# Kernel tuning notes

Measured on AMD Instinct MI355X. Metric: run time of the kernel, lower is better.

Reference implementation:

```python
import jax, jax.numpy as jnp
import numpy as np

H = 4                 # num_heads
GATE_NORM = 16.0      # gate_logit_normalizer
EPS = 1e-5            # RMSNorm eps


def setup_inputs() -> dict:
    key = jax.random.key(0)
    ks = jax.random.split(key, 12)
    B, T, D = 8, 4096, 1024
    Dk_total, Dv_total, Dlow = D // 2, D, 16

    def w(k, shape, fan_in):
        return jax.random.normal(k, shape, dtype=jnp.float32) * (fan_in ** -0.5)

    return {
        "x": jax.random.normal(ks[0], (B, T, D), dtype=jnp.float32),
        "Wq": w(ks[1], (D, Dk_total), D),
        "Wk": w(ks[2], (D, Dk_total), D),
        "Wv": w(ks[3], (D, Dv_total), D),
        "gk_w1": w(ks[4], (D, Dlow), D),
        "gk_w2": w(ks[5], (Dlow, Dk_total), Dlow),
        "gk_b2": jnp.zeros((Dk_total,), dtype=jnp.float32),
        "Wg": w(ks[6], (D, Dv_total), D),
        "g_norm_w": jnp.ones((Dv_total // H,), dtype=jnp.float32),
        "Wo": w(ks[7], (Dv_total, D), Dv_total),
    }


def _gla_forward(x, Wq, Wk, Wv, gk_w1, gk_w2, gk_b2, Wg, g_norm_w, Wo):
    B, T, D = x.shape
    Dk = Wq.shape[1] // H
    Dv = Wv.shape[1] // H

    q = (x @ Wq).reshape(B, T, H, Dk) * (Dk ** -0.5)
    k = (x @ Wk).reshape(B, T, H, Dk)
    v = (x @ Wv).reshape(B, T, H, Dv)
    # low-rank gate logits -> log-space decay gk (<= 0)
    gk = jax.nn.log_sigmoid((x @ gk_w1) @ gk_w2 + gk_b2) / GATE_NORM
    gk = gk.reshape(B, T, H, Dk)

    # recurrent gated linear attention:
    #   S_t = exp(gk_t)[:, None] * S_{t-1} + k_t^T v_t ;  o_t = q_t @ S_t
    def step(S, qkvg):
        qt, kt, vt, gt = qkvg          # each [B, H, Dk|Dv]
        S = jnp.exp(gt)[..., None] * S + kt[..., None] * vt[..., None, :]
        ot = jnp.einsum("bhk,bhkv->bhv", qt, S)
        return S, ot

    S0 = jnp.zeros((B, H, Dk, Dv), dtype=x.dtype)
    tm = lambda a: jnp.swapaxes(a, 0, 1)  # [B,T,...] -> [T,B,...]
    _, o = jax.lax.scan(step, S0, (tm(q), tm(k), tm(v), tm(gk)))
    o = jnp.swapaxes(o, 0, 1)            # [B, T, H, Dv]

    # output gate: RMSNorm(o) * swish(g), per head
    g = (x @ Wg).reshape(B, T, H, Dv)
    o = o * jax.lax.rsqrt(jnp.mean(o * o, axis=-1, keepdims=True) + EPS) * g_norm_w
    o = o * (g * jax.nn.sigmoid(g))
    return o.reshape(B, T, H * Dv) @ Wo


def reference(x, Wq, Wk, Wv, gk_w1, gk_w2, gk_b2, Wg, g_norm_w, Wo):
    return _gla_forward(x, Wq, Wk, Wv, gk_w1, gk_w2, gk_b2, Wg, g_norm_w, Wo)
```

## Files before the change

### kernel.cpp

```cpp
#include <hip/hip_runtime.h>
#include <hip/hip_bf16.h>
#include <cstdint>
#include <cstddef>

typedef __hip_bfloat16 bf16;
typedef __attribute__((ext_vector_type(8))) short short8;
typedef __attribute__((ext_vector_type(4))) float floatx4;

__device__ __forceinline__ void gload_lds16(const void* g, void* l) {
  __builtin_amdgcn_global_load_lds(
      (__attribute__((address_space(1))) void*)(uintptr_t)g,
      (__attribute__((address_space(3))) void*)l, 16, 0, 0);
}

__device__ __forceinline__ short f2bbits(float f) {
  bf16 h = __float2bfloat16(f);
  return __builtin_bit_cast(short, h);
}
__device__ __forceinline__ float b2f(short s) {
  return __bfloat162float(__builtin_bit_cast(bf16, s));
}

__global__ __launch_bounds__(256) void convert_x(const float* __restrict__ x,
                                                 bf16* __restrict__ xb) {
  size_t i = ((size_t)blockIdx.x * 256 + threadIdx.x) * 8;
  float4 f0 = *(const float4*)(x + i);
  float4 f1 = *(const float4*)(x + i + 4);
  short8 r;
  r[0] = f2bbits(f0.x); r[1] = f2bbits(f0.y); r[2] = f2bbits(f0.z); r[3] = f2bbits(f0.w);
  r[4] = f2bbits(f1.x); r[5] = f2bbits(f1.y); r[6] = f2bbits(f1.z); r[7] = f2bbits(f1.w);
  *(short8*)(xb + i) = r;
}

__global__ __launch_bounds__(256) void transpose_w(const float* __restrict__ src,
                                                   bf16* __restrict__ dst, int cols) {
  __shared__ float tile[32][33];
  int n0 = blockIdx.x * 32, k0 = blockIdx.y * 32;
  int tx = threadIdx.x & 31, ty = threadIdx.x >> 5;
#pragma unroll
  for (int i = 0; i < 32; i += 8) {
    int kk = k0 + ty + i, nn = n0 + tx;
    tile[ty + i][tx] = (nn < cols) ? src[(size_t)kk * cols + nn] : 0.0f;
  }
  __syncthreads();
#pragma unroll
  for (int i = 0; i < 32; i += 8) {
    int nn = n0 + ty + i, kk = k0 + tx;
    if (nn < cols) dst[(size_t)nn * 1024 + kk] = __float2bfloat16(tile[tx][ty + i]);
  }
}

__global__ __launch_bounds__(256, 2) void gemm128(
    const bf16* __restrict__ A, const bf16* __restrict__ Bt, int K, int mode,
    float* __restrict__ oq, float* __restrict__ okk, bf16* __restrict__ ov,
    bf16* __restrict__ ogg, float* __restrict__ oo) {
  __shared__ __align__(16) bf16 sA[128 * 32];
  __shared__ __align__(16) bf16 sB[128 * 32];
  const int tid = threadIdx.x;
  const int wave = tid >> 6, lane = tid & 63;
  const int n0 = blockIdx.x * 128, m0 = blockIdx.y * 128;
  const int wm = (wave & 1) * 64, wn = (wave >> 1) * 64;
  const int srow = lane >> 2, scol = (lane & 3) * 8;
  floatx4 acc[4][4] = {};
  const int kIters = K >> 5;
  for (int kt = 0; kt < kIters; ++kt) {
    if (kt) __syncthreads();
    const int kO = (kt << 5) + scol;
#pragma unroll
    for (int c2 = 0; c2 < 2; ++c2) {
      const int chunk = wave * 2 + c2;
      gload_lds16(A + (size_t)(m0 + chunk * 16 + srow) * K + kO, &sA[chunk * 512]);
      gload_lds16(Bt + (size_t)(n0 + chunk * 16 + srow) * K + kO, &sB[chunk * 512]);
    }
    __syncthreads();
    const int l15 = lane & 15, q8 = (lane >> 4) * 8;
    short8 af[4], bfr[4];
#pragma unroll
    for (int i = 0; i < 4; ++i) af[i] = *(const short8*)&sA[(wm + i * 16 + l15) * 32 + q8];
#pragma unroll
    for (int j = 0; j < 4; ++j) bfr[j] = *(const short8*)&sB[(wn + j * 16 + l15) * 32 + q8];
#pragma unroll
    for (int i = 0; i < 4; ++i)
#pragma unroll
      for (int j = 0; j < 4; ++j)
        acc[i][j] = __builtin_amdgcn_mfma_f32_16x16x32_bf16(af[i], bfr[j], acc[i][j], 0, 0, 0);
  }
  const int l15 = lane & 15, rq = (lane >> 4) * 4;
#pragma unroll
  for (int i = 0; i < 4; ++i) {
#pragma unroll
    for (int j = 0; j < 4; ++j) {
      const int n = n0 + wn + j * 16 + l15;
#pragma unroll
      for (int r = 0; r < 4; ++r) {
        const int m = m0 + wm + i * 16 + rq + r;
        const float val = acc[i][j][r];
        if (mode == 1) {
          oo[(size_t)m * 1024 + n] = val;
        } else {
          if (n < 512)       oq[(size_t)m * 512 + n] = val * 0.08838834764831845f;
          else if (n < 1024) okk[(size_t)m * 512 + (n - 512)] = val;
          else if (n < 2048) ov[(size_t)m * 1024 + (n - 1024)] = __float2bfloat16(val);
          else               ogg[(size_t)m * 1024 + (n - 2048)] = __float2bfloat16(val);
        }
      }
    }
  }
}

__global__ __launch_bounds__(256) void gate_decay2(const float* __restrict__ x,
                                                   const float* __restrict__ w1,
                                                   const float* __restrict__ w2,
                                                   const float* __restrict__ b2,
                                                   float* __restrict__ gkout) {
  __shared__ float sp[256];
  __shared__ float sz[16];
  const int m = blockIdx.x, tid = threadIdx.x;
  const int j = tid & 15, dpart = tid >> 4;
  const float* xr = x + (size_t)m * 1024 + dpart * 64;
  float acc = 0.f;
#pragma unroll 8
  for (int e = 0; e < 64; ++e) acc = fmaf(xr[e], w1[(dpart * 64 + e) * 16 + j], acc);
  sp[tid] = acc;
  __syncthreads();
  if (tid < 16) {
    float s = 0.f;
#pragma unroll
    for (int p = 0; p < 16; ++p) s += sp[p * 16 + tid];
    sz[tid] = s;
  }
  __syncthreads();
#pragma unroll
  for (int u = 0; u < 2; ++u) {
    const int n = tid + u * 256;
    float t = b2[n];
#pragma unroll
    for (int jj = 0; jj < 16; ++jj) t = fmaf(sz[jj], w2[jj * 512 + n], t);
    const float ls = fminf(t, 0.f) - log1pf(__expf(-fabsf(t)));
    gkout[(size_t)m * 512 + n] = ls * 0.0625f;
  }
}

__global__ __launch_bounds__(128) void chunk_prep(
    const float* __restrict__ q, const float* __restrict__ k,
    const float* __restrict__ gk, bf16* __restrict__ qt,
    bf16* __restrict__ kt, float* __restrict__ dtot) {
  const int cid = blockIdx.x;
  const int c = cid & 63, h = (cid >> 6) & 3, b = cid >> 8;
  const int d = threadIdx.x;
  const size_t rowbase = ((size_t)(b * 4096 + c * 64)) * 512 + h * 128 + d;
  const size_t obase = (size_t)cid * 8192 + d;
  float bsum = 0.f;
  for (int i = 0; i < 64; ++i) {
    const size_t src = rowbase + (size_t)i * 512;
    bsum += gk[src];
    qt[obase + (size_t)i * 128] = __float2bfloat16(q[src] * __expf(bsum));
    kt[obase + (size_t)i * 128] = __float2bfloat16(k[src] * __expf(-bsum));
  }
  dtot[cid * 128 + d] = __expf(bsum);
}

__global__ __launch_bounds__(256) void chunk_intra(
    const bf16* __restrict__ qt, const bf16* __restrict__ kt,
    const float* __restrict__ dtot, const bf16* __restrict__ v,
    bf16* __restrict__ oi, bf16* __restrict__ ut) {
  __shared__ __align__(16) short lA[64 * 72];
  __shared__ __align__(16) short stg[27648];
  short* sQ = stg;
  short* sK = stg + 8704;
  short* sVT = stg;
  short* sKhT = stg + 18432;
  const int cid = blockIdx.x;
  const int c = cid & 63, h = (cid >> 6) & 3, b = cid >> 8;
  const int tid = threadIdx.x, wv = tid >> 6, lane = tid & 63;
  const int l15 = lane & 15, q8 = (lane >> 4) * 8, rq = (lane >> 4) * 4;

  {
    const int row = tid >> 2, seg = (tid & 3) * 32;
    const size_t src = (size_t)cid * 8192 + row * 128 + seg;
    const short8* qs = (const short8*)(qt + src);
    const short8* ks = (const short8*)(kt + src);
    short8* qd = (short8*)&sQ[row * 136 + seg];
    short8* kd = (short8*)&sK[row * 136 + seg];
#pragma unroll
    for (int t = 0; t < 4; ++t) { qd[t] = qs[t]; kd[t] = ks[t]; }
  }
  __syncthreads();
  {
    short8 af[4];
#pragma unroll
    for (int kf = 0; kf < 4; ++kf)
      af[kf] = *(const short8*)&sQ[(wv * 16 + l15) * 136 + kf * 32 + q8];
#pragma unroll
    for (int nt = 0; nt < 4; ++nt) {
      floatx4 accA = {0.f, 0.f, 0.f, 0.f};
#pragma unroll
      for (int kf = 0; kf < 4; ++kf) {
        short8 bfr = *(const short8*)&sK[(nt * 16 + l15) * 136 + kf * 32 + q8];
        accA = __builtin_amdgcn_mfma_f32_16x16x32_bf16(af[kf], bfr, accA, 0, 0, 0);
      }
#pragma unroll
      for (int r = 0; r < 4; ++r) {
        const int i = wv * 16 + rq + r, jj = nt * 16 + l15;
        lA[i * 72 + jj] = f2bbits(jj <= i ? accA[r] : 0.f);
      }
    }
  }
  __syncthreads();
  {
#pragma unroll
    for (int e = 0; e < 8; ++e) {
      const int idx = tid + e * 256;
      const int jj = idx >> 5, n0 = (idx & 31) * 8;
      short8 vv = *(const short8*)(v + ((size_t)(b * 4096 + c * 64 + jj)) * 1024 + h * 256 + n0);
#pragma unroll
      for (int t = 0; t < 8; ++t) sVT[(n0 + t) * 72 + jj] = vv[t];
    }
#pragma unroll
    for (int e = 0; e < 4; ++e) {
      const int idx = tid + e * 256;
      const int jj = idx >> 4, d0 = (idx & 15) * 8;
      short8 kk = *(const short8*)(kt + (size_t)cid * 8192 + jj * 128 + d0);
#pragma unroll
      for (int t = 0; t < 8; ++t)
        sKhT[(d0 + t) * 72 + jj] = f2bbits(b2f(kk[t]) * dtot[cid * 128 + d0 + t]);
    }
  }
  __syncthreads();
  {
    short8 aA0 = *(const short8*)&lA[(wv * 16 + l15) * 72 + q8];
    short8 aA1 = *(const short8*)&lA[(wv * 16 + l15) * 72 + 32 + q8];
#pragma unroll
    for (int nt = 0; nt < 16; ++nt) {
      short8 b0 = *(const short8*)&sVT[(nt * 16 + l15) * 72 + q8];
      short8 b1 = *(const short8*)&sVT[(nt * 16 + l15) * 72 + 32 + q8];
      floatx4 acc = {0.f, 0.f, 0.f, 0.f};
      acc = __builtin_amdgcn_mfma_f32_16x16x32_bf16(aA0, b0, acc, 0, 0, 0);
      acc = __builtin_amdgcn_mfma_f32_16x16x32_bf16(aA1, b1, acc, 0, 0, 0);
#pragma unroll
      for (int r = 0; r < 4; ++r) {
        const int i = wv * 16 + rq + r;
        oi[(size_t)cid * 16384 + i * 256 + nt * 16 + l15] = __builtin_bit_cast(bf16, f2bbits(acc[r]));
      }
    }
  }
  {
    short8 aV[4][2];
#pragma unroll
    for (int mt = 0; mt < 4; ++mt) {
      aV[mt][0] = *(const short8*)&sVT[(wv * 64 + mt * 16 + l15) * 72 + q8];
      aV[mt][1] = *(const short8*)&sVT[(wv * 64 + mt * 16 + l15) * 72 + 32 + q8];
    }
#pragma unroll
    for (int nt = 0; nt < 8; ++nt) {
      short8 b0 = *(const short8*)&sKhT[(nt * 16 + l15) * 72 + q8];
      short8 b1 = *(const short8*)&sKhT[(nt * 16 + l15) * 72 + 32 + q8];
#pragma unroll
      for (int mt = 0; mt < 4; ++mt) {
        floatx4 acc = {0.f, 0.f, 0.f, 0.f};
        acc = __builtin_amdgcn_mfma_f32_16x16x32_bf16(aV[mt][0], b0, acc, 0, 0, 0);
        acc = __builtin_amdgcn_mfma_f32_16x16x32_bf16(aV[mt][1], b1, acc, 0, 0, 0);
#pragma unroll
        for (int r = 0; r < 4; ++r) {
          const int vr = wv * 64 + mt * 16 + rq + r;
          ut[(size_t)cid * 32768 + vr * 128 + nt * 16 + l15] = __builtin_bit_cast(bf16, f2bbits(acc[r]));
        }
      }
    }
  }
}

__global__ __launch_bounds__(256) void state_prop(
    bf16* __restrict__ su,
    const float* __restrict__ dtot) {
  const int ng = blockIdx.x, h = blockIdx.y, b = blockIdx.z;
  const int tid = threadIdx.x;
  const int nrow = ng * 32 + (tid >> 3), kseg = (tid & 7) * 16;
  const int cid0 = (b * 4 + h) * 64;
  const size_t off = (size_t)nrow * 128 + kseg;
  size_t a = (size_t)cid0 * 32768 + off;
  float S[16];
#pragma unroll
  for (int e = 0; e < 16; ++e) S[e] = 0.f;
  short8 u0 = *(const short8*)(su + a);
  short8 u1 = *(const short8*)(su + a + 8);
  for (int c = 0; c < 64; ++c) {
    short8 un0, un1;
    if (c < 63) {
      un0 = *(const short8*)(su + a + 32768);
      un1 = *(const short8*)(su + a + 32768 + 8);
    }
    const float4 d0 = *(const float4*)(dtot + (cid0 + c) * 128 + kseg);
    const float4 d1 = *(const float4*)(dtot + (cid0 + c) * 128 + kseg + 4);
    const float4 d2 = *(const float4*)(dtot + (cid0 + c) * 128 + kseg + 8);
    const float4 d3 = *(const float4*)(dtot + (cid0 + c) * 128 + kseg + 12);
    short8 s0, s1;
#pragma unroll
    for (int e = 0; e < 8; ++e) { s0[e] = f2bbits(S[e]); s1[e] = f2bbits(S[8 + e]); }
    *(short8*)(su + a) = s0;
    *(short8*)(su + a + 8) = s1;
    const float dd[16] = {d0.x, d0.y, d0.z, d0.w, d1.x, d1.y, d1.z, d1.w,
                          d2.x, d2.y, d2.z, d2.w, d3.x, d3.y, d3.z, d3.w};
#pragma unroll
    for (int e = 0; e < 8; ++e) S[e] = fmaf(dd[e], S[e], b2f(u0[e]));
#pragma unroll
    for (int e = 0; e < 8; ++e) S[8 + e] = fmaf(dd[8 + e], S[8 + e], b2f(u1[e]));
    u0 = un0; u1 = un1;
    a += 32768;
  }
}

__global__ __launch_bounds__(256, 2) void o_inter(
    const bf16* __restrict__ qt, const bf16* __restrict__ scb,
    const bf16* __restrict__ oi, bf16* __restrict__ opre) {
  __shared__ __align__(16) short sQ[64 * 136];
  const int cid = blockIdx.x;
  const int c = cid & 63, h = (cid >> 6) & 3, b = cid >> 8;
  const int tid = threadIdx.x, wv = tid >> 6, lane = tid & 63;
  const int l15 = lane & 15, q8 = (lane >> 4) * 8, rq = (lane >> 4) * 4;
  {
    const int row = tid >> 2, seg = (tid & 3) * 32;
    const short8* qs = (const short8*)(qt + (size_t)cid * 8192 + row * 128 + seg);
    short8* qd = (short8*)&sQ[row * 136 + seg];
#pragma unroll
    for (int t = 0; t < 4; ++t) qd[t] = qs[t];
  }
  __syncthreads();
  short8 af[4][4];
#pragma unroll
  for (int i = 0; i < 4; ++i)
#pragma unroll
    for (int kf = 0; kf < 4; ++kf)
      af[i][kf] = *(const short8*)&sQ[(i * 16 + l15) * 136 + kf * 32 + q8];
  floatx4 acc[4][4] = {};
#pragma unroll
  for (int j = 0; j < 4; ++j) {
#pragma unroll
    for (int kf = 0; kf < 4; ++kf) {
      short8 bfr = *(const short8*)(scb + (size_t)cid * 32768 +
                                    (size_t)(wv * 64 + j * 16 + l15) * 128 + kf * 32 + q8);
#pragma unroll
      for (int i = 0; i < 4; ++i)
        acc[i][j] = __builtin_amdgcn_mfma_f32_16x16x32_bf16(af[i][kf], bfr, acc[i][j], 0, 0, 0);
    }
  }
  const size_t rowg0 = (size_t)(b * 4096 + c * 64);
#pragma unroll
  for (int i = 0; i < 4; ++i) {
#pragma unroll
    for (int j = 0; j < 4; ++j) {
      const int col = wv * 64 + j * 16 + l15;
#pragma unroll
      for (int r = 0; r < 4; ++r) {
        const int row = i * 16 + rq + r;
        const float val = acc[i][j][r] +
            __bfloat162float(oi[(size_t)cid * 16384 + row * 256 + col]);
        opre[(rowg0 + row) * 1024 + h * 256 + col] = __float2bfloat16(val);
      }
    }
  }
}

__global__ __launch_bounds__(1024) void norm_gate(
    const bf16* __restrict__ o, const bf16* __restrict__ g,
    const float* __restrict__ gnw, bf16* __restrict__ og) {
  __shared__ float sp[16];
  const int tid = threadIdx.x;
  const size_t idx = (size_t)blockIdx.x * 1024 + tid;
  const float f = __bfloat162float(o[idx]);
  float ss = f * f;
#pragma unroll
  for (int mm = 1; mm <= 32; mm <<= 1) ss += __shfl_xor(ss, mm);
  if ((tid & 63) == 0) sp[tid >> 6] = ss;
  __syncthreads();
  const int h4 = (tid >> 8) * 4;
  const float ms = (sp[h4] + sp[h4 + 1] + sp[h4 + 2] + sp[h4 + 3]) * (1.0f / 256.0f);
  const float scale = rsqrtf(ms + 1e-5f) * gnw[tid & 255];
  const float gv = __bfloat162float(g[idx]);
  const float sw = gv * (1.0f / (1.0f + __expf(-gv)));
  og[idx] = __float2bfloat16(f * scale * sw);
}

extern "C" void kernel_launch(void* const* d_in, const int* in_sizes, int n_in,
                              void* d_out, int out_size, void* d_ws, size_t ws_size,
                              hipStream_t stream) {
  const float* x   = (const float*)d_in[0];
  const float* Wq  = (const float*)d_in[1];
  const float* Wk  = (const float*)d_in[2];
  const float* Wv  = (const float*)d_in[3];
  const float* gw1 = (const float*)d_in[4];
  const float* gw2 = (const float*)d_in[5];
  const float* gb2 = (const float*)d_in[6];
  const float* Wg  = (const float*)d_in[7];
  const float* gnw = (const float*)d_in[8];
  const float* Wo  = (const float*)d_in[9];
  float* out = (float*)d_out;

  const size_t Mi = 1048576;
  uint8_t* w = (uint8_t*)d_ws;
  bf16*  wallT = (bf16*)(w);
  bf16*  woT   = (bf16*)(w + 6 * Mi);
  float* dtot  = (float*)(w + 8 * Mi);
  bf16*  xb    = (bf16*)(w + 9 * Mi);
  bf16*  qt    = (bf16*)(w + 9 * Mi);
  bf16*  ktb   = (bf16*)(w + 41 * Mi);
  bf16*  ogat  = (bf16*)(w + 9 * Mi);
  float* qb    = (float*)(w + 73 * Mi);
  float* kb    = (float*)(w + 137 * Mi);
  bf16*  utb   = (bf16*)(w + 73 * Mi);
  float* gkb   = (float*)(w + 201 * Mi);
  bf16*  oib   = (bf16*)(w + 201 * Mi);
  bf16*  vb    = (bf16*)(w + 265 * Mi);
  bf16*  opre  = (bf16*)(w + 265 * Mi);
  bf16*  gb    = (bf16*)(w + 329 * Mi);

  convert_x<<<dim3(16384), 256, 0, stream>>>(x, xb);
  transpose_w<<<dim3(16, 32), 256, 0, stream>>>(Wq, wallT, 512);
  transpose_w<<<dim3(16, 32), 256, 0, stream>>>(Wk, wallT + (size_t)512 * 1024, 512);
  transpose_w<<<dim3(32, 32), 256, 0, stream>>>(Wv, wallT + (size_t)1024 * 1024, 1024);
  transpose_w<<<dim3(32, 32), 256, 0, stream>>>(Wg, wallT + (size_t)2048 * 1024, 1024);
  transpose_w<<<dim3(32, 32), 256, 0, stream>>>(Wo, woT, 1024);
  gemm128<<<dim3(24, 256), 256, 0, stream>>>(xb, wallT, 1024, 0, qb, kb, vb, gb, nullptr);
  gate_decay2<<<dim3(32768), 256, 0, stream>>>(x, gw1, gw2, gb2, gkb);
  chunk_prep<<<dim3(2048), 128, 0, stream>>>(qb, kb, gkb, qt, ktb, dtot);
  chunk_intra<<<dim3(2048), 256, 0, stream>>>(qt, ktb, dtot, vb, oib, utb);
  state_prop<<<dim3(8, 4, 8), 256, 0, stream>>>(utb, dtot);
  o_inter<<<dim3(2048), 256, 0, stream>>>(qt, utb, oib, opre);
  norm_gate<<<dim3(32768), 1024, 0, stream>>>(opre, gb, gnw, ogat);
  gemm128<<<dim3(8, 256), 256, 0, stream>>>(ogat, woT, 1024, 1, nullptr, nullptr, nullptr, nullptr, out);
}
```

Measured before the change: 1.228 ms.

## Replace 128x128 GEMM with 256x256 double-buffered, swizzled LDS pipelined GEMM

Both projection GEMMs move from a 128x128 tile, 4-wave kernel with a single LDS buffer to a 256x256 tile, 8-wave kernel. The new kernel uses 128 KB of dynamic LDS, double-buffered global-to-LDS loads interleaved with MFMA phases, an XOR-swizzled LDS layout to avoid bank conflicts, raised wave priority during MFMA, and a grouped block-index swizzle for L2 reuse. The aim is more data reuse per tile and hiding of global load latency behind compute. The cost is higher register and LDS pressure, which limits occupancy, plus a dependence on the exact barrier and vmcnt sequencing being correct.

Measured after the change: 1.190 ms. -3.1%, faster.

```diff
diff --git a/kernel.cpp b/kernel.cpp
--- a/kernel.cpp
+++ b/kernel.cpp
@@ -50,58 +50,142 @@
   }
 }
 
-__global__ __launch_bounds__(256, 2) void gemm128(
-    const bf16* __restrict__ A, const bf16* __restrict__ Bt, int K, int mode,
+#define BARR __builtin_amdgcn_s_barrier()
+#define WAITV(n) asm volatile("s_waitcnt vmcnt(" #n ")" ::: "memory")
+
+#define STA(buf, h, tau) do { \
+  gload_lds16(pA + (size_t)(h) * K64 + (size_t)(tau) * 64, \
+              &lds[(buf) * 16384 + (h) * 8192 + w * 512]); \
+  gload_lds16(pA + K128 + (size_t)(h) * K64 + (size_t)(tau) * 64, \
+              &lds[(buf) * 16384 + (h) * 8192 + 4096 + w * 512]); \
+} while (0)
+
+#define STB(buf, h, tau) do { \
+  gload_lds16(pB + (size_t)(h) * K32 + (size_t)(tau) * 64, \
+              &lds[32768 + (buf) * 16384 + (h) * 8192 + w * 512]); \
+  gload_lds16(pB + K128 + (size_t)(h) * K32 + (size_t)(tau) * 64, \
+              &lds[32768 + (buf) * 16384 + (h) * 8192 + 4096 + w * 512]); \
+} while (0)
+
+#define LDA(mh, buf) do { \
+  _Pragma("unroll") \
+  for (int mp = 0; mp < 4; ++mp) { \
+    const short* p_ = &lds[(buf) * 16384 + (mh) * 8192 + aRow + mp * 1024]; \
+    a[mp][0] = *(const short8*)(p_ + g0); \
+    a[mp][1] = *(const short8*)(p_ + g1); \
+  } \
+} while (0)
+
+#define LDB(nh, buf, d0, d1) do { \
+  const short* p_ = &lds[(buf) * 16384 + (nh) * 8192 + bRow]; \
+  d0[0] = *(const short8*)(p_ + g0); \
+  d0[1] = *(const short8*)(p_ + g1); \
+  d1[0] = *(const short8*)(p_ + 1024 + g0); \
+  d1[1] = *(const short8*)(p_ + 1024 + g1); \
+} while (0)
+
+#define MQ(MB, NB, d0, d1) do { \
+  __builtin_amdgcn_s_setprio(1); \
+  _Pragma("unroll") \
+  for (int mp = 0; mp < 4; ++mp) { \
+    acc[(MB) + mp][(NB)] = __builtin_amdgcn_mfma_f32_16x16x32_bf16(a[mp][0], d0[0], acc[(MB) + mp][(NB)], 0, 0, 0); \
+    acc[(MB) + mp][(NB)] = __builtin_amdgcn_mfma_f32_16x16x32_bf16(a[mp][1], d0[1], acc[(MB) + mp][(NB)], 0, 0, 0); \
+    acc[(MB) + mp][(NB) + 1] = __builtin_amdgcn_mfma_f32_16x16x32_bf16(a[mp][0], d1[0], acc[(MB) + mp][(NB) + 1], 0, 0, 0); \
+    acc[(MB) + mp][(NB) + 1] = __builtin_amdgcn_mfma_f32_16x16x32_bf16(a[mp][1], d1[1], acc[(MB) + mp][(NB) + 1], 0, 0, 0); \
+  } \
+  __builtin_amdgcn_s_setprio(0); \
+} while (0)
+
+__global__ __launch_bounds__(512, 2) void gemm256(
+    const bf16* __restrict__ A, const bf16* __restrict__ Bt, const int K,
+    const int nTN, const int mode,
     float* __restrict__ oq, float* __restrict__ okk, bf16* __restrict__ ov,
     bf16* __restrict__ ogg, float* __restrict__ oo) {
-  __shared__ __align__(16) bf16 sA[128 * 32];
-  __shared__ __align__(16) bf16 sB[128 * 32];
+  extern __shared__ __align__(16) short lds[];
   const int tid = threadIdx.x;
-  const int wave = tid >> 6, lane = tid & 63;
-  const int n0 = blockIdx.x * 128, m0 = blockIdx.y * 128;
-  const int wm = (wave & 1) * 64, wn = (wave >> 1) * 64;
-  const int srow = lane >> 2, scol = (lane & 3) * 8;
-  floatx4 acc[4][4] = {};
-  const int kIters = K >> 5;
-  for (int kt = 0; kt < kIters; ++kt) {
-    if (kt) __syncthreads();
-    const int kO = (kt << 5) + scol;
-#pragma unroll
-    for (int c2 = 0; c2 < 2; ++c2) {
-      const int chunk = wave * 2 + c2;
-      gload_lds16(A + (size_t)(m0 + chunk * 16 + srow) * K + kO, &sA[chunk * 512]);
-      gload_lds16(Bt + (size_t)(n0 + chunk * 16 + srow) * K + kO, &sB[chunk * 512]);
-    }
-    __syncthreads();
-    const int l15 = lane & 15, q8 = (lane >> 4) * 8;
-    short8 af[4], bfr[4];
-#pragma unroll
-    for (int i = 0; i < 4; ++i) af[i] = *(const short8*)&sA[(wm + i * 16 + l15) * 32 + q8];
-#pragma unroll
-    for (int j = 0; j < 4; ++j) bfr[j] = *(const short8*)&sB[(wn + j * 16 + l15) * 32 + q8];
-#pragma unroll
-    for (int i = 0; i < 4; ++i)
-#pragma unroll
-      for (int j = 0; j < 4; ++j)
-        acc[i][j] = __builtin_amdgcn_mfma_f32_16x16x32_bf16(af[i], bfr[j], acc[i][j], 0, 0, 0);
-  }
-  const int l15 = lane & 15, rq = (lane >> 4) * 4;
-#pragma unroll
-  for (int i = 0; i < 4; ++i) {
-#pragma unroll
-    for (int j = 0; j < 4; ++j) {
-      const int n = n0 + wn + j * 16 + l15;
+  const int w = tid >> 6, lane = tid & 63;
+  const int wr = w >> 2, wc = w & 3;
+  const int l15 = lane & 15, lq = lane >> 4;
+  const int e7 = lane & 7, l3 = lane >> 3;
+  const int gAp = (lane & 7) ^ l3;
+
+  const int cpx = (int)gridDim.x >> 3;
+  const int bid = blockIdx.x;
+  const int swz = (bid & 7) * cpx + (bid >> 3);
+  const int mt = swz / nTN, nt = swz - mt * nTN;
+  const int m0 = mt << 8, n0 = nt << 8;
+
+  const size_t K64 = (size_t)K * 64, K128 = (size_t)K * 128, K32 = (size_t)K * 32;
+  const bf16* pA = A + (size_t)(m0 + w * 8 + l3) * K + gAp * 8;
+  const bf16* pB = Bt + (size_t)(n0 + (w >> 2) * 64 + (w & 3) * 8 + l3) * K + gAp * 8;
+
+  const int g0 = ((lq ^ e7) & 7) * 8;
+  const int g1 = (((lq + 4) ^ e7) & 7) * 8;
+  const int aRow = (wr * 64 + l15) * 64;
+  const int bRow = 32768 + (wc * 32 + l15) * 64;
+
+  floatx4 acc[8][4] = {};
+  short8 a[4][2], bb0[2], bb1[2], bb2[2], bb3[2];
+
+  STA(0, 0, 0); STB(0, 0, 0); STB(0, 1, 0); STA(0, 1, 0);
+  STA(1, 0, 1); STB(1, 1, 1);
+  WAITV(4);
+  BARR;
+
+  const int nIter = K >> 7;
+  for (int t = 0; t < nIter; ++t) {
+    const bool nl = (t < nIter - 1);
+    const int t1 = 2 * t + 1, t2 = 2 * t + 2, t3 = 2 * t + 3;
+    LDA(0, 0); LDB(0, 0, bb0, bb1);
+    STA(1, 1, t1);
+    BARR; MQ(0, 0, bb0, bb1); BARR;
+    LDB(1, 0, bb2, bb3);
+    STB(1, 0, t1);
+    BARR; MQ(0, 2, bb2, bb3); BARR;
+    LDA(1, 0);
+    if (nl) STA(0, 0, t2);
+    BARR; MQ(4, 2, bb2, bb3); BARR;
+    LDB(0, 0, bb0, bb1);
+    if (nl) STB(0, 1, t2);
+    BARR; MQ(4, 0, bb0, bb1);
+    if (nl) { WAITV(4); } else { WAITV(0); }
+    BARR;
+    LDA(0, 1); LDB(0, 1, bb0, bb1);
+    if (nl) STA(0, 1, t2);
+    BARR; MQ(0, 0, bb0, bb1); BARR;
+    LDB(1, 1, bb2, bb3);
+    if (nl) STB(0, 0, t2);
+    BARR; MQ(0, 2, bb2, bb3); BARR;
+    LDA(1, 1);
+    if (nl) STA(1, 0, t3);
+    BARR; MQ(4, 2, bb2, bb3); BARR;
+    LDB(0, 1, bb0, bb1);
+    if (nl) STB(1, 1, t3);
+    BARR; MQ(4, 0, bb0, bb1);
+    if (nl) { WAITV(4); }
+    BARR;
+  }
+
+  const int rq = lq * 4;
+#pragma unroll
+  for (int m = 0; m < 8; ++m) {
+#pragma unroll
+    for (int n = 0; n < 4; ++n) {
+      const int col = n0 + wc * 64 + n * 16 + l15;
 #pragma unroll
       for (int r = 0; r < 4; ++r) {
-        const int m = m0 + wm + i * 16 + rq + r;
-        const float val = acc[i][j][r];
+        const size_t row = (size_t)(m0 + wr * 128 + m * 16 + rq + r);
+        const float val = acc[m][n][r];
         if (mode == 1) {
-          oo[(size_t)m * 1024 + n] = val;
+          oo[row * 1024 + col] = val;
+        } else if (col < 512) {
+          oq[row * 512 + col] = val * 0.08838834764831845f;
+        } else if (col < 1024) {
+          okk[row * 512 + (col - 512)] = val;
+        } else if (col < 2048) {
+          ov[row * 1024 + (col - 1024)] = __float2bfloat16(val);
         } else {
-          if (n < 512)       oq[(size_t)m * 512 + n] = val * 0.08838834764831845f;
-          else if (n < 1024) okk[(size_t)m * 512 + (n - 512)] = val;
-          else if (n < 2048) ov[(size_t)m * 1024 + (n - 1024)] = __float2bfloat16(val);
-          else               ogg[(size_t)m * 1024 + (n - 2048)] = __float2bfloat16(val);
+          ogg[row * 1024 + (col - 2048)] = __float2bfloat16(val);
         }
       }
     }
@@ -395,6 +479,13 @@
   const float* gnw = (const float*)d_in[8];
   const float* Wo  = (const float*)d_in[9];
   float* out = (float*)d_out;
+
+  static bool attr_set = false;
+  if (!attr_set) {
+    hipFuncSetAttribute(reinterpret_cast<const void*>(gemm256),
+                        hipFuncAttributeMaxDynamicSharedMemorySize, 131072);
+    attr_set = true;
+  }
 
   const size_t Mi = 1048576;
   uint8_t* w = (uint8_t*)d_ws;
@@ -420,12 +511,12 @@
   transpose_w<<<dim3(32, 32), 256, 0, stream>>>(Wv, wallT + (size_t)1024 * 1024, 1024);
   transpose_w<<<dim3(32, 32), 256, 0, stream>>>(Wg, wallT + (size_t)2048 * 1024, 1024);
   transpose_w<<<dim3(32, 32), 256, 0, stream>>>(Wo, woT, 1024);
-  gemm128<<<dim3(24, 256), 256, 0, stream>>>(xb, wallT, 1024, 0, qb, kb, vb, gb, nullptr);
+  gemm256<<<dim3(1536), 512, 131072, stream>>>(xb, wallT, 1024, 12, 0, qb, kb, vb, gb, nullptr);
   gate_decay2<<<dim3(32768), 256, 0, stream>>>(x, gw1, gw2, gb2, gkb);
   chunk_prep<<<dim3(2048), 128, 0, stream>>>(qb, kb, gkb, qt, ktb, dtot);
   chunk_intra<<<dim3(2048), 256, 0, stream>>>(qt, ktb, dtot, vb, oib, utb);
   state_prop<<<dim3(8, 4, 8), 256, 0, stream>>>(utb, dtot);
   o_inter<<<dim3(2048), 256, 0, stream>>>(qt, utb, oib, opre);
   norm_gate<<<dim3(32768), 1024, 0, stream>>>(opre, gb, gnw, ogat);
-  gemm128<<<dim3(8, 256), 256, 0, stream>>>(ogat, woT, 1024, 1, nullptr, nullptr, nullptr, nullptr, out);
-}
+  gemm256<<<dim3(512), 512, 131072, stream>>>(ogat, woT, 1024, 4, 1, nullptr, nullptr, nullptr, nullptr, out);
+}
```
